# Kernel tuning notes

Hardware: AMD Instinct MI355X
Metric: run time of the kernel (lower is better)

Reference implementation:

```python
import jax, jax.numpy as jnp
import numpy as np
from jax import lax

V_TH = 1.0  # spiking threshold (spikingjelly default)

# Heaviside spike with Rect surrogate gradient (width 1 around threshold)
@jax.custom_vjp
def spike(v):
    return (v >= V_TH).astype(v.dtype)

def _spike_fwd(v):
    return spike(v), v

def _spike_bwd(v, g):
    return (g * (jnp.abs(v - V_TH) < 0.5).astype(g.dtype),)

spike.defvjp(_spike_fwd, _spike_bwd)


def synapse_filter(x, inv_tau):
    # y[t] = y[t-1] * (1 - inv_tau) + x[t]   (spikingjelly SynapseFilter)
    decay = 1.0 - inv_tau
    def step(y, xt):
        y = y * decay + xt
        return y, y
    _, ys = lax.scan(step, jnp.zeros_like(x[0]), x)
    return ys


def lif_seq(x, tau):
    # LIFNode, decay_input=True, v_reset=0 (hard reset): v += (x - v)/tau
    inv_tau = 1.0 / tau
    def step(v, xt):
        v = v + (xt - v) * inv_tau
        s = spike(v)
        return v * (1.0 - s), s
    _, ss = lax.scan(step, jnp.zeros_like(x[0]), x)
    return ss


def if_seq(x):
    # IFNode, v_reset=0 (hard reset): v += x
    def step(v, xt):
        v = v + xt
        s = spike(v)
        return v * (1.0 - s), s
    _, ss = lax.scan(step, jnp.zeros_like(x[0]), x)
    return ss


def setup_inputs() -> dict:
    key = jax.random.key(0)
    ks = jax.random.split(key, 12)
    T, N, C, A = 32, 64, 512, 32
    F = [2048, 1024, 512]
    f32 = jnp.float32

    def lin_w(k, out_d, in_d):
        b = 1.0 / np.sqrt(in_d)
        return jax.random.uniform(k, (out_d, in_d), f32, -b, b)

    x = jax.random.uniform(ks[0], (T, N, 2, C), f32)  # (T,N,2,C) input currents
    w_sf_init = jnp.asarray(-np.log(10.0 - 1.0), f32)  # sigmoid(w)=1/tau, tau=10
    return {
        "x": x,
        "w_jeff": lin_w(ks[1], A, 2),        # JeffressLinear weight: 2 -> cc_acc
        "w_cc": lin_w(ks[2], 1, A),          # Linear(cc_acc, 1)
        "w_sf0": w_sf_init,
        "W1": lin_w(ks[3], F[0], C),
        "w_sf1": w_sf_init,
        "W2": lin_w(ks[4], F[1], F[0]),
        "w_sf2": w_sf_init,
        "W3": lin_w(ks[5], F[2], F[1]),
        "w_sf3": w_sf_init,
        "W_out": lin_w(ks[6], 1, F[2]),
        "b_out": jax.random.uniform(ks[7], (1,), f32, -1.0 / np.sqrt(F[2]), 1.0 / np.sqrt(F[2])),
    }


def reference(x, w_jeff, w_cc, w_sf0, W1, w_sf1, W2, w_sf2, W3, w_sf3, W_out, b_out):
    JEFF_TAU = 2.0
    LIF_TAU = 1.5
    # TransposeLayer((2,3)): (T,N,2,C) -> (T,N,C,2)
    y = jnp.swapaxes(x, 2, 3)
    # JeffressLinear(cc_acc, tau=2, bias=False): synapse low-pass then 2 -> cc_acc
    y = synapse_filter(y, 1.0 / JEFF_TAU)
    y = jnp.einsum('tnci,ai->tnca', y, w_jeff)
    # LIFNode(tau=1.5)
    y = lif_seq(y, LIF_TAU)
    # SynapseFilter(tau=10, learnable)
    y = synapse_filter(y, jax.nn.sigmoid(w_sf0))
    # Linear(cc_acc, 1) + Flatten(start_dim=2): (T,N,C,A) -> (T,N,C)
    y = jnp.einsum('tnca,oa->tnco', y, w_cc)[..., 0]
    # IFNode
    y = if_seq(y)
    # stacked [SynapseFilter, Linear, IFNode] blocks
    for w_sf, W in ((w_sf1, W1), (w_sf2, W2), (w_sf3, W3)):
        y = synapse_filter(y, jax.nn.sigmoid(w_sf))
        y = jnp.einsum('tnc,oc->tno', y, W)
        y = if_seq(y)
    # final Linear(feature_dims[-1], 1, bias=True)
    y = jnp.einsum('tnf,of->tno', y, W_out) + b_out
    # NonSpikingIFNode: v[t] = v[t-1] + x[t], output membrane potential
    out = jnp.cumsum(y, axis=0)  # (T, N, 1)
    return out
```

## Files before the change

kernel.cpp:

```cpp
#include <hip/hip_runtime.h>
#include <math.h>

#define T_STEPS 32
#define NB 64
#define CC 512
#define AA 32
#define MROWS (T_STEPS * NB)

typedef __attribute__((ext_vector_type(8)))  short bf16x8;
typedef __attribute__((ext_vector_type(16))) float f32x16;

__device__ __forceinline__ float sig_decay(const float* wp) {
    return 1.0f - 1.0f / (1.0f + expf(-wp[0]));
}

__device__ __forceinline__ unsigned short f2bf_rne(float f) {
    unsigned int u = __float_as_uint(f);
    u += 0x7FFF + ((u >> 16) & 1);
    return (unsigned short)(u >> 16);
}


__global__ __launch_bounds__(256) void pack_b_kernel(
    const float* __restrict__ W, unsigned short* __restrict__ out,
    int Nw, int Kw, int kshift)
{
    int i = blockIdx.x * 256 + threadIdx.x;
    int n = i >> kshift;
    int k = i & (Kw - 1);
    if (n >= Nw) return;
    float w = W[i];
    unsigned short h = f2bf_rne(w);
    float fh = __uint_as_float((unsigned int)h << 16);
    float r = w - fh;
    unsigned short m = f2bf_rne(r);
    float fm = __uint_as_float((unsigned int)m << 16);
    unsigned short l = f2bf_rne(r - fm);
    unsigned short vals[3] = {h, m, l};
    const int NT = Nw >> 5, KS = Kw >> 4;
    int L = (n & 31) + 32 * ((k >> 3) & 1);
#pragma unroll
    for (int p = 0; p < 3; p++) {
        size_t chunk = ((size_t)(p * NT + (n >> 5)) * KS + (k >> 4)) * 64 + L;
        out[chunk * 8 + (k & 7)] = vals[p];
    }
}

__global__ __launch_bounds__(256) void front_kernel(
    const float* __restrict__ x, const float* __restrict__ w_jeff,
    const float* __restrict__ w_cc, const float* __restrict__ w_sf0,
    const float* __restrict__ w_sf1,
    unsigned short* __restrict__ spike_out, float* __restrict__ filt_out)
{
    __shared__ float wj[2 * AA];
    __shared__ float wcc[AA];
    int tid = threadIdx.x;
    if (tid < 2 * AA) wj[tid] = w_jeff[tid];
    if (tid < AA) wcc[tid] = w_cc[tid];
    __syncthreads();

    int g = blockIdx.x * 256 + tid;
    int n = g >> 9;
    int c = g & (CC - 1);

    const float inv_lif = 1.0f / 1.5f;
    float d0 = sig_decay(w_sf0);
    float d1 = sig_decay(w_sf1);

    float s0 = 0.f, s1 = 0.f, v6 = 0.f, u1 = 0.f;
    float v[AA], u[AA];
#pragma unroll
    for (int a = 0; a < AA; a++) { v[a] = 0.f; u[a] = 0.f; }

    const int pL = (n & 31) + 32 * ((c >> 3) & 1);
    const int pks = c >> 4;
    const int pj = c & 7;

    for (int t = 0; t < T_STEPS; t++) {
        const float* xp = x + (size_t)((t * NB + n) * 2) * CC + c;
        s0 = s0 * 0.5f + xp[0];
        s1 = s1 * 0.5f + xp[CC];
        float acc = 0.f;
#pragma unroll
        for (int a = 0; a < AA; a++) {
            float z  = wj[2 * a] * s0 + wj[2 * a + 1] * s1;
            float vv = v[a] + (z - v[a]) * inv_lif;
            bool  sp = vv >= 1.0f;
            v[a] = sp ? 0.0f : vv;
            float uu = u[a] * d0 + (sp ? 1.0f : 0.0f);
            u[a] = uu;
            acc += wcc[a] * uu;
        }
        v6 += acc;
        bool sp6 = v6 >= 1.0f;
        v6 = sp6 ? 0.0f : v6;
        if (spike_out) {
            int mt = (t * NB + n) >> 5;
            size_t adr = (((size_t)mt * 32 + pks) * 64 + pL) * 8 + pj;
            spike_out[adr] = sp6 ? (unsigned short)0x3F80 : (unsigned short)0;
        } else {
            u1 = u1 * d1 + (sp6 ? 1.0f : 0.0f);
            filt_out[(size_t)(t * NB + n) * CC + c] = u1;
        }
    }
}

template <int NPARTS>
__global__ __launch_bounds__(256) void if_spike_kernel(
    const float* __restrict__ G, size_t partStride,
    const float* __restrict__ w_sf_in, int F, int fshift,
    unsigned short* __restrict__ out_bf, float* __restrict__ out_f32)
{
    constexpr int TT = 16 / NPARTS;
    constexpr int NTILES = T_STEPS / TT;

    int gid = blockIdx.x * 256 + threadIdx.x;
    int n = gid >> fshift;
    int f = gid & (F - 1);
    const int NT = F >> 5;
    const int NF = NB * F;
    float dz = sig_decay(w_sf_in);

    size_t base = ((size_t)(n >> 5) * NT + (f >> 5)) * 1024
                + (size_t)(n & 31) * 32 + (f & 31);
    const size_t tstride = (size_t)2 * NT * 1024;

    float buf[2][NPARTS][TT];
    auto pf = [&](int b, int tile) {
#pragma unroll
        for (int p = 0; p < NPARTS; p++)
#pragma unroll
            for (int j = 0; j < TT; j++)
                buf[b][p][j] = G[(size_t)p * partStride + base
                               + (size_t)(tile * TT + j) * tstride];
    };

    const int pL = (n & 31) + 32 * ((f >> 3) & 1);
    const int KS = F >> 4;

    pf(0, 0);
    float zf = 0.f, v = 0.f;
#pragma unroll
    for (int tile = 0; tile < NTILES; tile++) {
        const int b = tile & 1;
        if (tile + 1 < NTILES) pf(b ^ 1, tile + 1);
        __builtin_amdgcn_sched_barrier(0);
#pragma unroll
        for (int j = 0; j < TT; j++) {
            int t = tile * TT + j;
            float gsum = buf[b][0][j];
#pragma unroll
            for (int p = 1; p < NPARTS; p++) gsum += buf[b][p][j];
            zf = zf * dz + gsum;
            v += zf;
            bool sp = v >= 1.0f;
            v = sp ? 0.0f : v;
            if (out_bf) {
                int mt = 2 * t + (n >> 5);
                size_t adr = (((size_t)mt * KS + (f >> 4)) * 64 + pL) * 8 + (f & 7);
                out_bf[adr] = sp ? (unsigned short)0x3F80 : (unsigned short)0;
            } else {
                out_f32[(size_t)t * NF + gid] = sp ? 1.0f : 0.0f;
            }
        }
        __builtin_amdgcn_sched_barrier(0);
    }
}

__global__ __launch_bounds__(512, 2) void bgemm(
    const unsigned short* __restrict__ Ap,
    const unsigned short* __restrict__ Bp,
    float* __restrict__ C,
    int N, int K_total, int K_per)
{
    const int NT = N >> 5, KS = K_total >> 4;
    __shared__ uint4 sh[2][1792];

    const int tid = threadIdx.x;
    const int wv  = tid >> 6;
    const int L   = tid & 63;
    const int bm32 = blockIdx.x * 4;
    const int bn32 = blockIdx.y * 8;
    const int ks0  = (blockIdx.z * K_per) >> 4;
    const int nk   = K_per >> 4;

    f32x16 acc[4];
#pragma unroll
    for (int i = 0; i < 4; i++)
#pragma unroll
        for (int r = 0; r < 16; r++) acc[i][r] = 0.f;

    const uint4* A4 = (const uint4*)Ap;
    const uint4* B4 = (const uint4*)Bp;
    const int ntl = tid >> 6;
    const int cL  = tid & 63;

    uint4 pa, pb0, pb1, pb2;
    auto gload = [&](int ks) {
        if (tid < 256)
            pa = A4[((size_t)(bm32 + (tid >> 6)) * KS + ks) * 64 + (tid & 63)];
        pb0 = B4[((size_t)(0 * NT + bn32 + ntl) * KS + ks) * 64 + cL];
        pb1 = B4[((size_t)(1 * NT + bn32 + ntl) * KS + ks) * 64 + cL];
        pb2 = B4[((size_t)(2 * NT + bn32 + ntl) * KS + ks) * 64 + cL];
    };
    auto lwrite = [&](int b) {
        if (tid < 256) sh[b][tid] = pa;
        sh[b][256 + tid] = pb0;
        sh[b][256 + 512 + tid] = pb1;
        sh[b][256 + 1024 + tid] = pb2;
    };

    bf16x8 af[4], bf[3];
    auto rfrags = [&](int b) {
#pragma unroll
        for (int i = 0; i < 4; i++)
            af[i] = *(const bf16x8*)&sh[b][i * 64 + L];
#pragma unroll
        for (int p = 0; p < 3; p++)
            bf[p] = *(const bf16x8*)&sh[b][256 + (p * 8 + wv) * 64 + L];
    };

    gload(ks0);
    lwrite(0);
    if (nk > 1) gload(ks0 + 1);
    __syncthreads();
    rfrags(0);

    for (int kt = 0; kt < nk; kt++) {
        if (kt + 1 < nk) lwrite((kt + 1) & 1);
        if (kt + 2 < nk) gload(ks0 + kt + 2);
#pragma unroll
        for (int p = 0; p < 3; p++)
#pragma unroll
            for (int i = 0; i < 4; i++)
                acc[i] = __builtin_amdgcn_mfma_f32_32x32x16_bf16(
                    af[i], bf[p], acc[i], 0, 0, 0);
        if (kt + 1 < nk) {
            __syncthreads();
            rfrags((kt + 1) & 1);
        }
    }

    float* Cp = C + (size_t)blockIdx.z * ((size_t)MROWS * N);
    const int col = L & 31, rbase = 4 * (L >> 5);
#pragma unroll
    for (int i = 0; i < 4; i++) {
        size_t tb = ((size_t)(bm32 + i) * NT + (bn32 + wv)) * 1024;
#pragma unroll
        for (int r = 0; r < 16; r++) {
            int row = (r & 3) + 8 * (r >> 2) + rbase;
            Cp[tb + row * 32 + col] = acc[i][r];
        }
    }
}

__global__ __launch_bounds__(256) void if_filter_kernel(
    float* __restrict__ buf, size_t partStride, int nparts,
    const float* __restrict__ w_sf, int F)
{
    int tid = blockIdx.x * 256 + threadIdx.x;
    const int NF = NB * F;
    bool  filt = (w_sf != nullptr);
    float d = filt ? sig_decay(w_sf) : 0.0f;
    float v = 0.f, u = 0.f;
    for (int t = 0; t < T_STEPS; t++) {
        size_t off = (size_t)t * NF + tid;
        float zt = buf[off];
        for (int p = 1; p < nparts; p++) zt += buf[p * partStride + off];
        v += zt;
        bool sp = v >= 1.0f;
        v = sp ? 0.0f : v;
        float s = sp ? 1.0f : 0.0f;
        if (filt) { u = u * d + s; buf[off] = u; }
        else      { buf[off] = s; }
    }
}

__global__ __launch_bounds__(256) void gemm_nt(
    const float* __restrict__ A, const float* __restrict__ B,
    float* __restrict__ C, int M, int N, int K_total, int K_per)
{
    constexpr int BM = 64, BN = 64, BK = 32;
    __shared__ float As[BK][BM + 4];
    __shared__ float Bs[BK][BN + 4];
    const int tid = threadIdx.x;
    const int tx  = tid & 15;
    const int ty  = tid >> 4;
    const int bm  = blockIdx.y * BM;
    const int bn  = blockIdx.x * BN;
    const int kbeg = blockIdx.z * K_per;
    float acc[4][4];
#pragma unroll
    for (int i = 0; i < 4; i++)
#pragma unroll
        for (int j = 0; j < 4; j++) acc[i][j] = 0.f;
    const int lrow = tid >> 3;
    const int lkq  = tid & 7;
    for (int kt = 0; kt < K_per; kt += BK) {
        int k0 = kbeg + kt;
        __syncthreads();
#pragma unroll
        for (int i = 0; i < 2; i++) {
            int row = lrow + i * 32;
            float4 av = *(const float4*)(A + (size_t)(bm + row) * K_total + k0 + lkq * 4);
            As[lkq * 4 + 0][row] = av.x;
            As[lkq * 4 + 1][row] = av.y;
            As[lkq * 4 + 2][row] = av.z;
            As[lkq * 4 + 3][row] = av.w;
            float4 bv = *(const float4*)(B + (size_t)(bn + row) * K_total + k0 + lkq * 4);
            Bs[lkq * 4 + 0][row] = bv.x;
            Bs[lkq * 4 + 1][row] = bv.y;
            Bs[lkq * 4 + 2][row] = bv.z;
            Bs[lkq * 4 + 3][row] = bv.w;
        }
        __syncthreads();
#pragma unroll
        for (int kk = 0; kk < BK; kk++) {
            float4 a0 = *(const float4*)&As[kk][ty * 4];
            float4 b0 = *(const float4*)&Bs[kk][tx * 4];
            float ar[4] = {a0.x, a0.y, a0.z, a0.w};
            float br[4] = {b0.x, b0.y, b0.z, b0.w};
#pragma unroll
            for (int i = 0; i < 4; i++)
#pragma unroll
                for (int j = 0; j < 4; j++) acc[i][j] += ar[i] * br[j];
        }
    }
    float* Cp = C + (size_t)blockIdx.z * (size_t)M * N;
#pragma unroll
    for (int i = 0; i < 4; i++) {
        float4 o;
        o.x = acc[i][0]; o.y = acc[i][1]; o.z = acc[i][2]; o.w = acc[i][3];
        *(float4*)(Cp + (size_t)(bm + ty * 4 + i) * N + bn + tx * 4) = o;
    }
}

__global__ __launch_bounds__(64) void final_kernel(
    const float* __restrict__ y15, const float* __restrict__ W_out,
    const float* __restrict__ b_out, float* __restrict__ out)
{
    int n = blockIdx.x;
    int lane = threadIdx.x;
    float w[8];
#pragma unroll
    for (int j = 0; j < 8; j++) w[j] = W_out[lane + j * 64];
    float b = b_out[0];
    float cum = 0.f;
    for (int t = 0; t < T_STEPS; t++) {
        const float* yp = y15 + (size_t)(t * NB + n) * 512;
        float p = 0.f;
#pragma unroll
        for (int j = 0; j < 8; j++) p += yp[lane + j * 64] * w[j];
#pragma unroll
        for (int off = 32; off > 0; off >>= 1) p += __shfl_down(p, off);
        if (lane == 0) {
            cum += p + b;
            out[t * NB + n] = cum;
        }
    }
}

extern "C" void kernel_launch(void* const* d_in, const int* in_sizes, int n_in,
                              void* d_out, int out_size, void* d_ws, size_t ws_size,
                              hipStream_t stream) {
    (void)in_sizes; (void)n_in; (void)out_size;
    const float* x      = (const float*)d_in[0];
    const float* w_jeff = (const float*)d_in[1];
    const float* w_cc   = (const float*)d_in[2];
    const float* w_sf0  = (const float*)d_in[3];
    const float* W1     = (const float*)d_in[4];
    const float* w_sf1  = (const float*)d_in[5];
    const float* W2     = (const float*)d_in[6];
    const float* w_sf2  = (const float*)d_in[7];
    const float* W3     = (const float*)d_in[8];
    const float* w_sf3  = (const float*)d_in[9];
    const float* W_out  = (const float*)d_in[10];
    const float* b_out  = (const float*)d_in[11];
    float* out = (float*)d_out;
    const int M = MROWS;

    const size_t nW1 = (size_t)2048 * 512, nW2 = (size_t)1024 * 2048, nW3 = (size_t)512 * 1024;
    size_t need = 3 * (nW1 + nW2 + nW3) * 2
                + (size_t)M * 512 * 2
                + (size_t)2 * M * 2048 * 4
                + (size_t)M * 2048 * 2
                + (size_t)M * 1024 * 2
                + (size_t)M * 512 * 4;

    if (ws_size >= need) {
        unsigned short* Bp1 = (unsigned short*)d_ws;
        unsigned short* Bp2 = Bp1 + 3 * nW1;
        unsigned short* Bp3 = Bp2 + 3 * nW2;
        unsigned short* s6  = Bp3 + 3 * nW3;
        float* G   = (float*)(s6 + (size_t)M * 512);
        unsigned short* s8  = (unsigned short*)(G + (size_t)2 * M * 2048);
        unsigned short* s10 = s8 + (size_t)M * 2048;
        float* s12 = (float*)(s10 + (size_t)M * 1024);

        pack_b_kernel<<<(int)(nW1 / 256), 256, 0, stream>>>(W1, Bp1, 2048, 512, 9);
        pack_b_kernel<<<(int)(nW2 / 256), 256, 0, stream>>>(W2, Bp2, 1024, 2048, 11);
        pack_b_kernel<<<(int)(nW3 / 256), 256, 0, stream>>>(W3, Bp3, 512, 1024, 10);

        front_kernel<<<NB * CC / 256, 256, 0, stream>>>(
            x, w_jeff, w_cc, w_sf0, w_sf1, s6, nullptr);

        bgemm<<<dim3(16, 8, 2), 512, 0, stream>>>(s6, Bp1, G, 2048, 512, 256);
        if_spike_kernel<2><<<NB * 2048 / 256, 256, 0, stream>>>(
            G, (size_t)M * 2048, w_sf1, 2048, 11, s8, nullptr);

        bgemm<<<dim3(16, 4, 4), 512, 0, stream>>>(s8, Bp2, G, 1024, 2048, 512);
        if_spike_kernel<4><<<NB * 1024 / 256, 256, 0, stream>>>(
            G, (size_t)M * 1024, w_sf2, 1024, 10, s10, nullptr);

        bgemm<<<dim3(16, 2, 8), 512, 0, stream>>>(s10, Bp3, G, 512, 1024, 128);
        if_spike_kernel<8><<<NB * 512 / 256, 256, 0, stream>>>(
            G, (size_t)M * 512, w_sf3, 512, 9, nullptr, s12);

        final_kernel<<<NB, 64, 0, stream>>>(s12, W_out, b_out, out);
    } else {
        float* y7  = (float*)d_ws;
        float* z1  = y7 + (size_t)M * 512;
        float* z2p = z1 + (size_t)M * 2048;
        float* z3p = z1;
        size_t need2 = ((size_t)M * 512 + (size_t)M * 2048 + 2 * (size_t)M * 1024) * 4;
        const int ksplit2 = (ws_size >= need2) ? 2 : 1;

        front_kernel<<<NB * CC / 256, 256, 0, stream>>>(
            x, w_jeff, w_cc, w_sf0, w_sf1, nullptr, y7);
        gemm_nt<<<dim3(2048 / 64, 2048 / 64, 1), 256, 0, stream>>>(
            y7, W1, z1, M, 2048, 512, 512);
        if_filter_kernel<<<NB * 2048 / 256, 256, 0, stream>>>(z1, 0, 1, w_sf2, 2048);
        gemm_nt<<<dim3(1024 / 64, 2048 / 64, ksplit2), 256, 0, stream>>>(
            z1, W2, z2p, M, 1024, 2048, 2048 / ksplit2);
        if_filter_kernel<<<NB * 1024 / 256, 256, 0, stream>>>(
            z2p, (size_t)M * 1024, ksplit2, w_sf3, 1024);
        gemm_nt<<<dim3(512 / 64, 2048 / 64, 4), 256, 0, stream>>>(
            z2p, W3, z3p, M, 512, 1024, 1024 / 4);
        if_filter_kernel<<<NB * 512 / 256, 256, 0, stream>>>(
            z3p, (size_t)M * 512, 4, nullptr, 512);
        final_kernel<<<NB, 64, 0, stream>>>(z3p, W_out, b_out, out);
    }
}
```

Before: 246.2 us.

## Load B fragments directly to registers in bgemm and merge weight pack kernels

Result: faster. 226.6 us (-8.0%).

```diff
diff --git a/kernel.cpp b/kernel.cpp
--- a/kernel.cpp
+++ b/kernel.cpp
@@ -21,15 +21,17 @@
 }
 
 
-__global__ __launch_bounds__(256) void pack_b_kernel(
+#define NW1 (2048 * 512)
+#define NW2 (1024 * 2048)
+#define NW3 (512 * 1024)
+
+__device__ __forceinline__ void pack_one(
     const float* __restrict__ W, unsigned short* __restrict__ out,
-    int Nw, int Kw, int kshift)
-{
-    int i = blockIdx.x * 256 + threadIdx.x;
-    int n = i >> kshift;
-    int k = i & (Kw - 1);
-    if (n >= Nw) return;
-    float w = W[i];
+    int idx, int Nw, int Kw, int kshift)
+{
+    int n = idx >> kshift;
+    int k = idx & (Kw - 1);
+    float w = W[idx];
     unsigned short h = f2bf_rne(w);
     float fh = __uint_as_float((unsigned int)h << 16);
     float r = w - fh;
@@ -43,6 +45,22 @@
     for (int p = 0; p < 3; p++) {
         size_t chunk = ((size_t)(p * NT + (n >> 5)) * KS + (k >> 4)) * 64 + L;
         out[chunk * 8 + (k & 7)] = vals[p];
+    }
+}
+
+__global__ __launch_bounds__(256) void pack_all_kernel(
+    const float* __restrict__ W1, const float* __restrict__ W2,
+    const float* __restrict__ W3,
+    unsigned short* __restrict__ B1, unsigned short* __restrict__ B2,
+    unsigned short* __restrict__ B3)
+{
+    int i = blockIdx.x * 256 + threadIdx.x;
+    if (i < NW1) {
+        pack_one(W1, B1, i, 2048, 512, 9);
+    } else if (i < NW1 + NW2) {
+        pack_one(W2, B2, i - NW1, 1024, 2048, 11);
+    } else if (i < NW1 + NW2 + NW3) {
+        pack_one(W3, B3, i - NW1 - NW2, 512, 1024, 10);
     }
 }
 
@@ -167,20 +185,20 @@
     }
 }
 
-__global__ __launch_bounds__(512, 2) void bgemm(
+__global__ __launch_bounds__(256, 2) void bgemm(
     const unsigned short* __restrict__ Ap,
     const unsigned short* __restrict__ Bp,
     float* __restrict__ C,
     int N, int K_total, int K_per)
 {
     const int NT = N >> 5, KS = K_total >> 4;
-    __shared__ uint4 sh[2][1792];
+    __shared__ bf16x8 shA[2][256];
 
     const int tid = threadIdx.x;
     const int wv  = tid >> 6;
     const int L   = tid & 63;
     const int bm32 = blockIdx.x * 4;
-    const int bn32 = blockIdx.y * 8;
+    const int bn32 = blockIdx.y * 4;
     const int ks0  = (blockIdx.z * K_per) >> 4;
     const int nk   = K_per >> 4;
 
@@ -190,56 +208,62 @@
 #pragma unroll
         for (int r = 0; r < 16; r++) acc[i][r] = 0.f;
 
-    const uint4* A4 = (const uint4*)Ap;
-    const uint4* B4 = (const uint4*)Bp;
-    const int ntl = tid >> 6;
-    const int cL  = tid & 63;
-
-    uint4 pa, pb0, pb1, pb2;
-    auto gload = [&](int ks) {
-        if (tid < 256)
-            pa = A4[((size_t)(bm32 + (tid >> 6)) * KS + ks) * 64 + (tid & 63)];
-        pb0 = B4[((size_t)(0 * NT + bn32 + ntl) * KS + ks) * 64 + cL];
-        pb1 = B4[((size_t)(1 * NT + bn32 + ntl) * KS + ks) * 64 + cL];
-        pb2 = B4[((size_t)(2 * NT + bn32 + ntl) * KS + ks) * 64 + cL];
+    const bf16x8* A8 = (const bf16x8*)Ap;
+    const bf16x8* B8 = (const bf16x8*)Bp;
+
+    bf16x8 pa;
+    auto gloadA = [&](int ks) {
+        pa = A8[((size_t)(bm32 + wv) * KS + ks) * 64 + L];
     };
-    auto lwrite = [&](int b) {
-        if (tid < 256) sh[b][tid] = pa;
-        sh[b][256 + tid] = pb0;
-        sh[b][256 + 512 + tid] = pb1;
-        sh[b][256 + 1024 + tid] = pb2;
+    auto lwriteA = [&](int b) { shA[b][tid] = pa; };
+
+    bf16x8 pb0[3], pb1[3];
+    auto gloadB = [&](int ks, bf16x8* pbuf) {
+#pragma unroll
+        for (int p = 0; p < 3; p++)
+            pbuf[p] = B8[((size_t)(p * NT + bn32 + wv) * KS + ks) * 64 + L];
     };
 
-    bf16x8 af[4], bf[3];
-    auto rfrags = [&](int b) {
+    bf16x8 af[4];
+    auto rfragsA = [&](int b) {
 #pragma unroll
         for (int i = 0; i < 4; i++)
-            af[i] = *(const bf16x8*)&sh[b][i * 64 + L];
-#pragma unroll
-        for (int p = 0; p < 3; p++)
-            bf[p] = *(const bf16x8*)&sh[b][256 + (p * 8 + wv) * 64 + L];
+            af[i] = shA[b][i * 64 + L];
     };
 
-    gload(ks0);
-    lwrite(0);
-    if (nk > 1) gload(ks0 + 1);
+    gloadA(ks0);
+    gloadB(ks0, pb0);
+    lwriteA(0);
+    gloadA(ks0 + 1);
+    gloadB(ks0 + 1, pb1);
     __syncthreads();
-    rfrags(0);
-
-    for (int kt = 0; kt < nk; kt++) {
-        if (kt + 1 < nk) lwrite((kt + 1) & 1);
-        if (kt + 2 < nk) gload(ks0 + kt + 2);
-#pragma unroll
-        for (int p = 0; p < 3; p++)
-#pragma unroll
-            for (int i = 0; i < 4; i++)
-                acc[i] = __builtin_amdgcn_mfma_f32_32x32x16_bf16(
-                    af[i], bf[p], acc[i], 0, 0, 0);
-        if (kt + 1 < nk) {
-            __syncthreads();
-            rfrags((kt + 1) & 1);
-        }
-    }
+    rfragsA(0);
+
+#define BG_STAGE(KT, CB, PB)                                                  \
+    {                                                                         \
+        bf16x8 b0 = PB[0], b1 = PB[1], b2 = PB[2];                            \
+        if ((KT) + 1 < nk) lwriteA((CB) ^ 1);           \
+        if ((KT) + 2 < nk) {                                                  \
+            gloadA(ks0 + (KT) + 2);                                           \
+            gloadB(ks0 + (KT) + 2, PB);                                       \
+        }                                                                     \
+        _Pragma("unroll")                                                     \
+        for (int i = 0; i < 4; i++)                                           \
+            acc[i] = __builtin_amdgcn_mfma_f32_32x32x16_bf16(af[i], b0, acc[i], 0, 0, 0); \
+        _Pragma("unroll")                                                     \
+        for (int i = 0; i < 4; i++)                                           \
+            acc[i] = __builtin_amdgcn_mfma_f32_32x32x16_bf16(af[i], b1, acc[i], 0, 0, 0); \
+        _Pragma("unroll")                                                     \
+        for (int i = 0; i < 4; i++)                                           \
+            acc[i] = __builtin_amdgcn_mfma_f32_32x32x16_bf16(af[i], b2, acc[i], 0, 0, 0); \
+        if ((KT) + 1 < nk) { __syncthreads(); rfragsA((CB) ^ 1); }            \
+    }
+
+    for (int kt = 0; kt < nk; kt += 2) {
+        BG_STAGE(kt, 0, pb0);
+        BG_STAGE(kt + 1, 1, pb1);
+    }
+#undef BG_STAGE
 
     float* Cp = C + (size_t)blockIdx.z * ((size_t)MROWS * N);
     const int col = L & 31, rbase = 4 * (L >> 5);
@@ -379,7 +403,7 @@
     float* out = (float*)d_out;
     const int M = MROWS;
 
-    const size_t nW1 = (size_t)2048 * 512, nW2 = (size_t)1024 * 2048, nW3 = (size_t)512 * 1024;
+    const size_t nW1 = NW1, nW2 = NW2, nW3 = NW3;
     size_t need = 3 * (nW1 + nW2 + nW3) * 2
                 + (size_t)M * 512 * 2
                 + (size_t)2 * M * 2048 * 4
@@ -397,22 +421,21 @@
         unsigned short* s10 = s8 + (size_t)M * 2048;
         float* s12 = (float*)(s10 + (size_t)M * 1024);
 
-        pack_b_kernel<<<(int)(nW1 / 256), 256, 0, stream>>>(W1, Bp1, 2048, 512, 9);
-        pack_b_kernel<<<(int)(nW2 / 256), 256, 0, stream>>>(W2, Bp2, 1024, 2048, 11);
-        pack_b_kernel<<<(int)(nW3 / 256), 256, 0, stream>>>(W3, Bp3, 512, 1024, 10);
+        pack_all_kernel<<<(int)((nW1 + nW2 + nW3 + 255) / 256), 256, 0, stream>>>(
+            W1, W2, W3, Bp1, Bp2, Bp3);
 
         front_kernel<<<NB * CC / 256, 256, 0, stream>>>(
             x, w_jeff, w_cc, w_sf0, w_sf1, s6, nullptr);
 
-        bgemm<<<dim3(16, 8, 2), 512, 0, stream>>>(s6, Bp1, G, 2048, 512, 256);
+        bgemm<<<dim3(16, 16, 2), 256, 0, stream>>>(s6, Bp1, G, 2048, 512, 256);
         if_spike_kernel<2><<<NB * 2048 / 256, 256, 0, stream>>>(
             G, (size_t)M * 2048, w_sf1, 2048, 11, s8, nullptr);
 
-        bgemm<<<dim3(16, 4, 4), 512, 0, stream>>>(s8, Bp2, G, 1024, 2048, 512);
+        bgemm<<<dim3(16, 8, 4), 256, 0, stream>>>(s8, Bp2, G, 1024, 2048, 512);
         if_spike_kernel<4><<<NB * 1024 / 256, 256, 0, stream>>>(
             G, (size_t)M * 1024, w_sf2, 1024, 10, s10, nullptr);
 
-        bgemm<<<dim3(16, 2, 8), 512, 0, stream>>>(s10, Bp3, G, 512, 1024, 128);
+        bgemm<<<dim3(16, 4, 8), 256, 0, stream>>>(s10, Bp3, G, 512, 1024, 128);
         if_spike_kernel<8><<<NB * 512 / 256, 256, 0, stream>>>(
             G, (size_t)M * 512, w_sf3, 512, 9, nullptr, s12);
 
```
